# Kernel tuning notes

Measured on AMD Instinct MI355X. Metric: run time of the kernel, lower is better.

Reference implementation:

```python
import jax, jax.numpy as jnp
import numpy as np

INNER_DIM = 64
NUM_LABELS = 16
BIG_NEG = 1e12


def setup_inputs() -> dict:
    key = jax.random.key(0)
    k1, k2 = jax.random.split(key)
    B, S, H = 8, 512, 768
    sequence_output = jax.random.normal(k1, (B, S, H), dtype=jnp.float32)
    attention_mask = jnp.ones((B, S), dtype=jnp.int32)
    W = jax.random.normal(k2, (NUM_LABELS * INNER_DIM * 2, H), dtype=jnp.float32) * 0.02
    b = jnp.zeros((NUM_LABELS * INNER_DIM * 2,), dtype=jnp.float32)
    return {"sequence_output": sequence_output, "attention_mask": attention_mask,
            "W": W, "b": b}


def _rope_sincos(seq_len, dim, dtype):
    # interleaved sinusoidal embedding: [sin0,cos0,sin1,cos1,...]
    pos = jnp.arange(seq_len, dtype=dtype)[:, None]              # [S,1]
    idx = jnp.arange(dim // 2, dtype=dtype)
    theta = jnp.power(jnp.asarray(1000.0, dtype), -2.0 * idx / dim)
    ang = pos * theta                                            # [S, dim/2]
    # cos_pos/sin_pos after repeat_interleave(2): [c0,c0,c1,c1,...]
    cos_pos = jnp.repeat(jnp.cos(ang), 2, axis=-1)               # [S, dim]
    sin_pos = jnp.repeat(jnp.sin(ang), 2, axis=-1)               # [S, dim]
    return sin_pos, cos_pos


def _rotate_half_interleaved(x):
    # stack([-x[...,1::2], x[...,::2]], -1).reshape(x.shape)
    x2 = jnp.stack([-x[..., 1::2], x[..., ::2]], axis=-1)
    return x2.reshape(x.shape)


def reference(sequence_output, attention_mask, W, b):
    B, S, H = sequence_output.shape
    L, D = NUM_LABELS, INNER_DIM
    # dense projection then split into per-label q/k: [B,S,L,2D]
    out = (sequence_output @ W.T + b).reshape(B, S, L, 2 * D)
    qw, kw = out[..., :D], out[..., D:]                          # [B,S,L,D]

    sin_pos, cos_pos = _rope_sincos(S, D, sequence_output.dtype)
    cos_pos = cos_pos[None, :, None, :]                          # [1,S,1,D]
    sin_pos = sin_pos[None, :, None, :]
    qw = qw * cos_pos + _rotate_half_interleaved(qw) * sin_pos
    kw = kw * cos_pos + _rotate_half_interleaved(kw) * sin_pos

    logits = jnp.einsum('bmhd,bnhd->bhmn', qw, kw)               # [B,L,S,S]

    pad = attention_mask.astype(logits.dtype)[:, None, None, :]  # [B,1,1,S]
    logits = logits * pad - (1.0 - pad) * BIG_NEG

    tril = jnp.tril(jnp.ones((S, S), dtype=logits.dtype), -1)    # strictly lower
    logits = logits - tril * BIG_NEG
    return logits / (D ** 0.5)
```

## Files before the change

kernel.cpp:

```cpp
#include <hip/hip_runtime.h>
#include <hip/hip_bf16.h>

typedef __bf16 bf16;
typedef __attribute__((ext_vector_type(8))) __bf16 bf16x8;
typedef __attribute__((ext_vector_type(4))) float f32x4;

#define BIG_NEG 1000000000000.0f
#define NEG_LOG_STEP 0.21586735253866545f

static __device__ inline uint2 pack4_bf16(float4 v) {
    union { bf16 h[4]; uint2 u; } t;
    t.h[0] = (bf16)v.x; t.h[1] = (bf16)v.y; t.h[2] = (bf16)v.z; t.h[3] = (bf16)v.w;
    return t.u;
}

__global__ __launch_bounds__(256) void proj_rope_kernel(
    const float* __restrict__ X, const float* __restrict__ W,
    const float* __restrict__ bias,
    bf16* __restrict__ q_ws, bf16* __restrict__ k_ws)
{
    const int K = 768;
    __shared__ __align__(16) bf16 As[128][40];
    __shared__ __align__(16) bf16 Bs[128][40];

    const int tid  = threadIdx.x;
    const int lane = tid & 63;
    const int wave = tid >> 6;
    const int wr   = wave >> 1;
    const int wc   = wave & 1;
    const int brow = blockIdx.x * 128;
    const int bcol = blockIdx.y * 128;
    const int lane15 = lane & 15;
    const int kq = (lane >> 4) * 8;

    f32x4 acc[4][4] = {};

    for (int k0 = 0; k0 < K; k0 += 32) {
        #pragma unroll
        for (int pass = 0; pass < 4; ++pass) {
            int e   = (pass * 256 + tid) * 4;
            int row = e >> 5;
            int col = e & 31;
            float4 xa = *reinterpret_cast<const float4*>(&X[(size_t)(brow + row) * K + k0 + col]);
            *reinterpret_cast<uint2*>(&As[row][col]) = pack4_bf16(xa);
            float4 wa = *reinterpret_cast<const float4*>(&W[(size_t)(bcol + row) * K + k0 + col]);
            *reinterpret_cast<uint2*>(&Bs[row][col]) = pack4_bf16(wa);
        }
        __syncthreads();

        bf16x8 af[4], bfv[4];
        #pragma unroll
        for (int mf = 0; mf < 4; ++mf)
            af[mf] = *reinterpret_cast<bf16x8*>(&As[wr * 64 + mf * 16 + lane15][kq]);
        #pragma unroll
        for (int nf = 0; nf < 4; ++nf)
            bfv[nf] = *reinterpret_cast<bf16x8*>(&Bs[wc * 64 + nf * 16 + lane15][kq]);
        #pragma unroll
        for (int mf = 0; mf < 4; ++mf)
            #pragma unroll
            for (int nf = 0; nf < 4; ++nf)
                acc[mf][nf] = __builtin_amdgcn_mfma_f32_16x16x32_bf16(
                    af[mf], bfv[nf], acc[mf][nf], 0, 0, 0);
        __syncthreads();
    }

    const int rowbase = brow + wr * 64 + (lane >> 4) * 4;
    const int colbase = bcol + wc * 64;
    #pragma unroll
    for (int nf = 0; nf < 4; ++nf) {
        int n = colbase + nf * 16 + lane15;
        int d = n & 127;
        int l = n >> 7;
        int p = (d & 63) >> 1;
        float theta = __expf(-(float)p * NEG_LOG_STEP);
        float bn = bias[n];
        bool odd = (d & 1) != 0;
        bf16* dst = (d < 64) ? q_ws : k_ws;
        int dd = d & 63;
        #pragma unroll
        for (int mf = 0; mf < 4; ++mf) {
            f32x4 v4 = acc[mf][nf];
            #pragma unroll
            for (int r = 0; r < 4; ++r) {
                int m = rowbase + mf * 16 + r;
                float v  = v4[r] + bn;
                float pv = __shfl_xor(v, 1);
                int s = m & 511;
                int b = m >> 9;
                float ang = (float)s * theta;
                float sn, cs;
                __sincosf(ang, &sn, &cs);
                float o = odd ? (v * cs + pv * sn) : (v * cs - pv * sn);
                dst[(((size_t)(b * 16 + l) * 512) + s) * 64 + dd] = (bf16)o;
            }
        }
    }
}

__global__ __launch_bounds__(256) void attn_kernel(
    const bf16* __restrict__ q_ws, const bf16* __restrict__ k_ws,
    const int* __restrict__ mask, float* __restrict__ out)
{
    __shared__ __align__(16) bf16 Qs[128][72];
    __shared__ __align__(16) bf16 Ks[128][72];

    const int tid  = threadIdx.x;
    const int lane = tid & 63;
    const int wave = tid >> 6;
    const int wr   = wave >> 1;
    const int wc   = wave & 1;
    const int bl   = blockIdx.z;
    const int brow = blockIdx.x * 128;
    const int bcol = blockIdx.y * 128;
    const int lane15 = lane & 15;

    const bf16* qbase = q_ws + (size_t)bl * 512 * 64;
    const bf16* kbase = k_ws + (size_t)bl * 512 * 64;

    #pragma unroll
    for (int pass = 0; pass < 4; ++pass) {
        int e   = (pass * 256 + tid) * 8;
        int row = e >> 6;
        int col = e & 63;
        *reinterpret_cast<uint4*>(&Qs[row][col]) =
            *reinterpret_cast<const uint4*>(&qbase[(size_t)(brow + row) * 64 + col]);
        *reinterpret_cast<uint4*>(&Ks[row][col]) =
            *reinterpret_cast<const uint4*>(&kbase[(size_t)(bcol + row) * 64 + col]);
    }
    __syncthreads();

    f32x4 acc[4][4] = {};
    #pragma unroll
    for (int ks = 0; ks < 2; ++ks) {
        int kq = ks * 32 + (lane >> 4) * 8;
        bf16x8 af[4], bfv[4];
        #pragma unroll
        for (int mf = 0; mf < 4; ++mf)
            af[mf] = *reinterpret_cast<bf16x8*>(&Qs[wr * 64 + mf * 16 + lane15][kq]);
        #pragma unroll
        for (int nf = 0; nf < 4; ++nf)
            bfv[nf] = *reinterpret_cast<bf16x8*>(&Ks[wc * 64 + nf * 16 + lane15][kq]);
        #pragma unroll
        for (int mf = 0; mf < 4; ++mf)
            #pragma unroll
            for (int nf = 0; nf < 4; ++nf)
                acc[mf][nf] = __builtin_amdgcn_mfma_f32_16x16x32_bf16(
                    af[mf], bfv[nf], acc[mf][nf], 0, 0, 0);
    }

    const int b = bl >> 4;
    const int* mrow = mask + b * 512;
    const int rowbase = brow + wr * 64 + (lane >> 4) * 4;
    const int colbase = bcol + wc * 64;
    #pragma unroll
    for (int nf = 0; nf < 4; ++nf) {
        int n = colbase + nf * 16 + lane15;
        float pf = (float)mrow[n];
        float mterm = (1.0f - pf) * BIG_NEG;
        #pragma unroll
        for (int mf = 0; mf < 4; ++mf) {
            f32x4 v4 = acc[mf][nf];
            #pragma unroll
            for (int r = 0; r < 4; ++r) {
                int m = rowbase + mf * 16 + r;
                float v = v4[r] * pf - mterm - ((m > n) ? BIG_NEG : 0.0f);
                out[((size_t)bl * 512 + m) * 512 + n] = v * 0.125f;
            }
        }
    }
}

extern "C" void kernel_launch(void* const* d_in, const int* in_sizes, int n_in,
                              void* d_out, int out_size, void* d_ws, size_t ws_size,
                              hipStream_t stream) {
    const float* X    = (const float*)d_in[0];
    const int*   mask = (const int*)d_in[1];
    const float* W    = (const float*)d_in[2];
    const float* bias = (const float*)d_in[3];

    float* out = (float*)d_out;
    bf16* q_ws = (bf16*)d_ws;
    bf16* k_ws = q_ws + (size_t)8 * 16 * 512 * 64;

    proj_rope_kernel<<<dim3(32, 16), 256, 0, stream>>>(X, W, bias, q_ws, k_ws);
    attn_kernel<<<dim3(4, 4, 128), 256, 0, stream>>>(q_ws, k_ws, mask, out);
}
```

Before: 73.05 us.

## Pre-convert X and W to bf16 and stage GEMM tiles via direct global-to-LDS loads

```diff
diff --git a/kernel.cpp b/kernel.cpp
--- a/kernel.cpp
+++ b/kernel.cpp
@@ -7,6 +7,11 @@
 
 #define BIG_NEG 1000000000000.0f
 #define NEG_LOG_STEP 0.21586735253866545f
+
+#define GLOAD_LDS16(g, l)                                                     \
+    __builtin_amdgcn_global_load_lds(                                         \
+        (const __attribute__((address_space(1))) void*)(g),                   \
+        (__attribute__((address_space(3))) void*)(l), 16, 0, 0)
 
 static __device__ inline uint2 pack4_bf16(float4 v) {
     union { bf16 h[4]; uint2 u; } t;
@@ -14,14 +19,30 @@
     return t.u;
 }
 
+__global__ __launch_bounds__(256) void convert_kernel(
+    const float* __restrict__ X, const float* __restrict__ W,
+    bf16* __restrict__ Xb, bf16* __restrict__ Wb)
+{
+    const int NX8 = (8 * 512 * 768) / 8;
+    int idx = blockIdx.x * 256 + threadIdx.x;
+    const float* src; bf16* dst; int i;
+    if (idx < NX8) { src = X; dst = Xb; i = idx; }
+    else           { src = W; dst = Wb; i = idx - NX8; }
+    float4 a = reinterpret_cast<const float4*>(src)[i * 2];
+    float4 b = reinterpret_cast<const float4*>(src)[i * 2 + 1];
+    uint2 lo = pack4_bf16(a), hi = pack4_bf16(b);
+    uint4 o; o.x = lo.x; o.y = lo.y; o.z = hi.x; o.w = hi.y;
+    reinterpret_cast<uint4*>(dst)[i] = o;
+}
+
 __global__ __launch_bounds__(256) void proj_rope_kernel(
-    const float* __restrict__ X, const float* __restrict__ W,
+    const bf16* __restrict__ A, const bf16* __restrict__ B,
     const float* __restrict__ bias,
     bf16* __restrict__ q_ws, bf16* __restrict__ k_ws)
 {
     const int K = 768;
-    __shared__ __align__(16) bf16 As[128][40];
-    __shared__ __align__(16) bf16 Bs[128][40];
+    __shared__ __align__(16) bf16 As[128][32];
+    __shared__ __align__(16) bf16 Bs[128][32];
 
     const int tid  = threadIdx.x;
     const int lane = tid & 63;
@@ -32,19 +53,17 @@
     const int bcol = blockIdx.y * 128;
     const int lane15 = lane & 15;
     const int kq = (lane >> 4) * 8;
+    const int srow = lane >> 2;
+    const int scol = (lane & 3) * 8;
 
     f32x4 acc[4][4] = {};
 
     for (int k0 = 0; k0 < K; k0 += 32) {
         #pragma unroll
-        for (int pass = 0; pass < 4; ++pass) {
-            int e   = (pass * 256 + tid) * 4;
-            int row = e >> 5;
-            int col = e & 31;
-            float4 xa = *reinterpret_cast<const float4*>(&X[(size_t)(brow + row) * K + k0 + col]);
-            *reinterpret_cast<uint2*>(&As[row][col]) = pack4_bf16(xa);
-            float4 wa = *reinterpret_cast<const float4*>(&W[(size_t)(bcol + row) * K + k0 + col]);
-            *reinterpret_cast<uint2*>(&Bs[row][col]) = pack4_bf16(wa);
+        for (int p = 0; p < 2; ++p) {
+            int r0 = p * 64 + wave * 16;
+            GLOAD_LDS16(A + (size_t)(brow + r0 + srow) * K + k0 + scol, &As[r0][0]);
+            GLOAD_LDS16(B + (size_t)(bcol + r0 + srow) * K + k0 + scol, &Bs[r0][0]);
         }
         __syncthreads();
 
@@ -179,9 +198,16 @@
     const float* bias = (const float*)d_in[3];
 
     float* out = (float*)d_out;
+
     bf16* q_ws = (bf16*)d_ws;
     bf16* k_ws = q_ws + (size_t)8 * 16 * 512 * 64;
 
-    proj_rope_kernel<<<dim3(32, 16), 256, 0, stream>>>(X, W, bias, q_ws, k_ws);
+    bf16* Xb = (bf16*)d_out;
+    bf16* Wb = Xb + (size_t)8 * 512 * 768;
+
+    const int NX8 = (8 * 512 * 768) / 8;
+    const int NW8 = (2048 * 768) / 8;
+    convert_kernel<<<(NX8 + NW8) / 256, 256, 0, stream>>>(X, W, Xb, Wb);
+    proj_rope_kernel<<<dim3(32, 16), 256, 0, stream>>>(Xb, Wb, bias, q_ws, k_ws);
     attn_kernel<<<dim3(4, 4, 128), 256, 0, stream>>>(q_ws, k_ws, mask, out);
 }
```

Result: faster. 67.20 us (-8.0%).
